# Kernel tuning notes

Hardware: AMD Instinct MI355X
Metric: run time of the kernel (lower is better)

## Reference

```python
import jax, jax.numpy as jnp
import numpy as np


def setup_inputs() -> dict:
    key = jax.random.key(0)
    ks = jax.random.split(key, 9)
    B, C, PF = 4, 256, 4096
    C8 = C // 8
    scale_qk = 1.0 / np.sqrt(C)
    return {
        "x": jax.random.normal(ks[0], (B, C, PF), dtype=jnp.float32),
        "xh1": jax.random.normal(ks[1], (B, C, PF), dtype=jnp.float32),
        "xl1": jax.random.normal(ks[2], (B, C, PF), dtype=jnp.float32),
        "Wq": jax.random.normal(ks[3], (C8, C), dtype=jnp.float32) * scale_qk,
        "bq": jnp.zeros((C8,), dtype=jnp.float32),
        "Wk": jax.random.normal(ks[4], (C8, C), dtype=jnp.float32) * scale_qk,
        "bk": jnp.zeros((C8,), dtype=jnp.float32),
        "Wv": jax.random.normal(ks[5], (C, C), dtype=jnp.float32) * scale_qk,
        "bv": jnp.zeros((C,), dtype=jnp.float32),
        "gamma1": jnp.array([0.5], dtype=jnp.float32),
        "gamma2": jnp.array([0.5], dtype=jnp.float32),
    }


def reference(x, xh1, xl1, Wq, bq, Wk, bk, Wv, bv, gamma1, gamma2):
    # x, xh1, xl1: (B, C, N) with N = H*W. Conv1x1 == channel-wise linear,
    # so the (B,C,H,W) reshape in the original is a no-op for the math.
    q = jnp.einsum("oc,bcn->bon", Wq, x) + bq[None, :, None]   # (B, C/8, N)
    k = jnp.einsum("oc,bcn->bon", Wk, x) + bk[None, :, None]   # (B, C/8, N)
    # energy[b, n, m] = q[:, :, n] . k[:, :, m]  (NO 1/sqrt(d) scale, as in source)
    energy = jnp.einsum("bcn,bcm->bnm", q, k)                  # (B, N, N)
    attention = jax.nn.softmax(energy, axis=-1)                # softmax over keys m
    vh = jnp.einsum("oc,bcn->bon", Wv, xh1) + bv[None, :, None]  # (B, C, N)
    vl = jnp.einsum("oc,bcn->bon", Wv, xl1) + bv[None, :, None]  # (B, C, N)
    # out = V @ attention^T : out[b, c, n] = sum_m vh[b, c, m] * attention[b, n, m]
    outh = jnp.einsum("bcm,bnm->bcn", vh, attention)
    outl = jnp.einsum("bcm,bnm->bcn", vl, attention)
    outh = xh1 * (gamma1 * outh)
    outl = xl1 * (gamma2 * outl)
    return outh, outl
```

## Files before the change

kernel.cpp:

```cpp
#include <hip/hip_runtime.h>
#include <math.h>

#define B_  4
#define C_  256
#define C8_ 32
#define N_  4096
#define NT_ 128

typedef __attribute__((ext_vector_type(8))) short          bf16x8;
typedef __attribute__((ext_vector_type(8))) unsigned short us8;
typedef __attribute__((ext_vector_type(4))) unsigned short us4;
typedef __attribute__((ext_vector_type(4))) float          f32x4;

__device__ inline unsigned short f2bf(float f) {
    unsigned u = __float_as_uint(f);
    u += 0x7FFFu + ((u >> 16) & 1u);
    return (unsigned short)(u >> 16);
}
__device__ inline void splitbf(float v, unsigned short& h, unsigned short& l) {
    unsigned short hh = f2bf(v);
    float hf = __uint_as_float((unsigned)hh << 16);
    h = hh; l = f2bf(v - hf);
}
__device__ inline bf16x8 asb(us8 v) { return __builtin_bit_cast(bf16x8, v); }

template<int MODE>
__global__ __launch_bounds__(256, 4) void proj_k(
    const float* __restrict__ Xa, const float* __restrict__ Xb,
    const float* __restrict__ Wa, const float* __restrict__ Wb,
    const float* __restrict__ ba, const float* __restrict__ bb,
    float* __restrict__ qt, float* __restrict__ ktt,
    unsigned short* __restrict__ vtc)
{
    __shared__ unsigned short XsH[32][66], XsL[32][66];
    __shared__ unsigned short WsH[64][40], WsL[64][40];

    const int m0 = blockIdx.x * 64;
    int b, s, cc0;
    const float* xptr;
    if (MODE == 0) { b = blockIdx.z; s = 0; cc0 = 0;
                     xptr = Xa + (size_t)b * C_ * N_; }
    else           { b = blockIdx.z & 3; s = blockIdx.z >> 2; cc0 = blockIdx.y * 64;
                     xptr = (s ? Xb : Xa) + (size_t)b * C_ * N_; }

    const int t = threadIdx.x;
    const int w = t >> 6, lane = t & 63, lr = lane & 15, ls = lane >> 4;

    f32x4 acc[4];
    #pragma unroll
    for (int i = 0; i < 4; ++i) acc[i] = (f32x4){0.f, 0.f, 0.f, 0.f};

    const int skk = t >> 3, smo = (t & 7) * 8;
    const int scc = t >> 2, sko = (t & 3) * 8;
    const float* wrow;
    if (MODE == 0) wrow = (scc < 32) ? (Wa + (size_t)scc * C_) : (Wb + (size_t)(scc - 32) * C_);
    else           wrow = Wa + (size_t)(cc0 + scc) * C_;

    for (int k0 = 0; k0 < C_; k0 += 32) {
        __syncthreads();
        {
            const float* src = xptr + (size_t)(k0 + skk) * N_ + m0 + smo;
            f32x4 a = *(const f32x4*)src, c = *(const f32x4*)(src + 4);
            unsigned short h[8], l[8];
            splitbf(a[0],h[0],l[0]); splitbf(a[1],h[1],l[1]);
            splitbf(a[2],h[2],l[2]); splitbf(a[3],h[3],l[3]);
            splitbf(c[0],h[4],l[4]); splitbf(c[1],h[5],l[5]);
            splitbf(c[2],h[6],l[6]); splitbf(c[3],h[7],l[7]);
            unsigned* dh = (unsigned*)&XsH[skk][smo];
            unsigned* dl = (unsigned*)&XsL[skk][smo];
            #pragma unroll
            for (int i = 0; i < 4; ++i) {
                dh[i] = (unsigned)h[2*i] | ((unsigned)h[2*i+1] << 16);
                dl[i] = (unsigned)l[2*i] | ((unsigned)l[2*i+1] << 16);
            }
        }
        {
            f32x4 a = *(const f32x4*)(wrow + k0 + sko);
            f32x4 c = *(const f32x4*)(wrow + k0 + sko + 4);
            us8 h, l; unsigned short hh, ll;
            splitbf(a[0],hh,ll); h[0]=hh; l[0]=ll;
            splitbf(a[1],hh,ll); h[1]=hh; l[1]=ll;
            splitbf(a[2],hh,ll); h[2]=hh; l[2]=ll;
            splitbf(a[3],hh,ll); h[3]=hh; l[3]=ll;
            splitbf(c[0],hh,ll); h[4]=hh; l[4]=ll;
            splitbf(c[1],hh,ll); h[5]=hh; l[5]=ll;
            splitbf(c[2],hh,ll); h[6]=hh; l[6]=ll;
            splitbf(c[3],hh,ll); h[7]=hh; l[7]=ll;
            *(us8*)&WsH[scc][sko] = h;
            *(us8*)&WsL[scc][sko] = l;
        }
        __syncthreads();
        us8 ahu, alu;
        #pragma unroll
        for (int j = 0; j < 8; ++j) {
            ahu[j] = XsH[ls*8 + j][w*16 + lr];
            alu[j] = XsL[ls*8 + j][w*16 + lr];
        }
        bf16x8 ah = asb(ahu), al = asb(alu);
        #pragma unroll
        for (int at = 0; at < 4; ++at) {
            bf16x8 bh = asb(*(const us8*)&WsH[at*16 + lr][ls*8]);
            bf16x8 bl = asb(*(const us8*)&WsL[at*16 + lr][ls*8]);
            acc[at] = __builtin_amdgcn_mfma_f32_16x16x32_bf16(ah, bh, acc[at], 0, 0, 0);
            acc[at] = __builtin_amdgcn_mfma_f32_16x16x32_bf16(ah, bl, acc[at], 0, 0, 0);
            acc[at] = __builtin_amdgcn_mfma_f32_16x16x32_bf16(al, bh, acc[at], 0, 0, 0);
        }
    }

    const int mrow = m0 + w*16 + ls*4;
    if (MODE == 0) {
        #pragma unroll
        for (int at = 0; at < 4; ++at) {
            const int cc = at*16 + lr;
            if (at < 2) {
                const float bia = ba[cc];
                #pragma unroll
                for (int r = 0; r < 4; ++r)
                    qt[((size_t)b * N_ + mrow + r) * C8_ + cc] = acc[at][r] + bia;
            } else {
                const float bia = bb[cc - 32];
                f32x4 o;
                #pragma unroll
                for (int r = 0; r < 4; ++r) o[r] = acc[at][r] + bia;
                *(f32x4*)&ktt[((size_t)b * C8_ + cc - 32) * N_ + mrow] = o;
            }
        }
    } else {
        #pragma unroll
        for (int at = 0; at < 4; ++at) {
            const int cc = cc0 + at*16 + lr;
            const float bia = ba[cc];
            us4 o;
            #pragma unroll
            for (int r = 0; r < 4; ++r) o[r] = f2bf(acc[at][r] + bia);
            *(us4*)&vtc[((size_t)b * 512 + s * 256 + cc) * N_ + mrow] = o;
        }
    }
}

__global__ __launch_bounds__(512, 4) void pv_k(
    const float* __restrict__ qt, const float* __restrict__ ktt,
    const unsigned short* __restrict__ vtc,
    const float* __restrict__ xh1, const float* __restrict__ xl1,
    const float* __restrict__ g1, const float* __restrict__ g2,
    float* __restrict__ out)
{
    __shared__ unsigned short KsH[2][32][34];
    __shared__ unsigned short KsL[2][32][34];
    __shared__ unsigned short Ps[32][40];
    __shared__ float          Zpart[2][32];

    const int orig = blockIdx.x;
    const int wg   = (orig & 7) * 64 + (orig >> 3);
    const int b    = wg >> 7;
    const int n0   = (wg & 127) * 32;

    const int t = threadIdx.x, w = t >> 6, lane = t & 63;
    const int lr = lane & 15, ls = lane >> 4;
    const int wn = w * 64;
    const bool ew = (w < 4);
    const int rt = (w >> 1) & 1, mt = w & 1;

    bf16x8 qh = {}, ql = {};
    if (ew) {
        const float* qrow = qt + ((size_t)b * N_ + n0 + rt*16 + lr) * C8_ + ls*8;
        f32x4 q0 = *(const f32x4*)qrow, q1 = *(const f32x4*)(qrow + 4);
        us8 hu, lu; unsigned short hh, ll;
        splitbf(q0[0],hh,ll); hu[0]=hh; lu[0]=ll;
        splitbf(q0[1],hh,ll); hu[1]=hh; lu[1]=ll;
        splitbf(q0[2],hh,ll); hu[2]=hh; lu[2]=ll;
        splitbf(q0[3],hh,ll); hu[3]=hh; lu[3]=ll;
        splitbf(q1[0],hh,ll); hu[4]=hh; lu[4]=ll;
        splitbf(q1[1],hh,ll); hu[5]=hh; lu[5]=ll;
        splitbf(q1[2],hh,ll); hu[6]=hh; lu[6]=ll;
        splitbf(q1[3],hh,ll); hu[7]=hh; lu[7]=ll;
        qh = asb(hu); ql = asb(lu);
    }

    f32x4 acc[2][4];
    #pragma unroll
    for (int i = 0; i < 2; ++i)
        #pragma unroll
        for (int j = 0; j < 4; ++j) acc[i][j] = (f32x4){0.f, 0.f, 0.f, 0.f};
    float zreg[4] = {0.f, 0.f, 0.f, 0.f};

    const unsigned short* vbase = vtc + (size_t)b * 512 * N_;
    const unsigned short* vp0 = vbase + (size_t)(wn +  0 + lr) * N_ + ls*8;
    const unsigned short* vp1 = vbase + (size_t)(wn + 16 + lr) * N_ + ls*8;
    const unsigned short* vp2 = vbase + (size_t)(wn + 32 + lr) * N_ + ls*8;
    const unsigned short* vp3 = vbase + (size_t)(wn + 48 + lr) * N_ + ls*8;

    const int ts = t - 256, kc = (ts & 255) >> 3, kmq = (ts & 7) * 4;
    const float* kptr = ktt + ((size_t)b * C8_ + kc) * N_ + kmq;

    us8 vA0, vA1, vA2, vA3, vB0, vB1, vB2, vB3;

    if (!ew) {
        f32x4 kv = *(const f32x4*)kptr;
        unsigned short h0,h1,h2,h3,l0,l1,l2,l3;
        splitbf(kv[0],h0,l0); splitbf(kv[1],h1,l1);
        splitbf(kv[2],h2,l2); splitbf(kv[3],h3,l3);
        unsigned* dh = (unsigned*)&KsH[0][kc][kmq];
        unsigned* dl = (unsigned*)&KsL[0][kc][kmq];
        dh[0] = (unsigned)h0 | ((unsigned)h1 << 16);
        dh[1] = (unsigned)h2 | ((unsigned)h3 << 16);
        dl[0] = (unsigned)l0 | ((unsigned)l1 << 16);
        dl[1] = (unsigned)l2 | ((unsigned)l3 << 16);
    }
    vA0 = *(const us8*)vp0; vA1 = *(const us8*)vp1;
    vA2 = *(const us8*)vp2; vA3 = *(const us8*)vp3;
    __syncthreads();

    auto body = [&](int CUR, int NXT, us8& VC0, us8& VC1, us8& VC2, us8& VC3,
                    us8& VN0, us8& VN1, us8& VN2, us8& VN3, int TILE) {
        const int tn = TILE + 1;
        f32x4 kreg;
        if (tn < NT_) {
            VN0 = *(const us8*)(vp0 + tn*32);
            VN1 = *(const us8*)(vp1 + tn*32);
            VN2 = *(const us8*)(vp2 + tn*32);
            VN3 = *(const us8*)(vp3 + tn*32);
            if (!ew) kreg = *(const f32x4*)(kptr + tn*32);
        }
        if (ew) {
            us8 khu, klu;
            #pragma unroll
            for (int j = 0; j < 8; ++j) {
                khu[j] = KsH[CUR][ls*8 + j][mt*16 + lr];
                klu[j] = KsL[CUR][ls*8 + j][mt*16 + lr];
            }
            bf16x8 kh = asb(khu), kl = asb(klu);
            f32x4 ea = (f32x4){0.f, 0.f, 0.f, 0.f};
            ea = __builtin_amdgcn_mfma_f32_16x16x32_bf16(qh, kh, ea, 0, 0, 0);
            ea = __builtin_amdgcn_mfma_f32_16x16x32_bf16(qh, kl, ea, 0, 0, 0);
            ea = __builtin_amdgcn_mfma_f32_16x16x32_bf16(ql, kh, ea, 0, 0, 0);
            #pragma unroll
            for (int r = 0; r < 4; ++r) {
                float pe = __expf(ea[r] - 20.f);
                zreg[r] += pe;
                Ps[rt*16 + ls*4 + r][mt*16 + lr] = f2bf(pe);
            }
        }
        __syncthreads();
        {
            bf16x8 pa0 = asb(*(const us8*)&Ps[lr][ls*8]);
            bf16x8 pa1 = asb(*(const us8*)&Ps[16 + lr][ls*8]);
            bf16x8 v0 = asb(VC0), v1 = asb(VC1), v2 = asb(VC2), v3 = asb(VC3);
            acc[0][0] = __builtin_amdgcn_mfma_f32_16x16x32_bf16(pa0, v0, acc[0][0], 0,0,0);
            acc[1][0] = __builtin_amdgcn_mfma_f32_16x16x32_bf16(pa1, v0, acc[1][0], 0,0,0);
            acc[0][1] = __builtin_amdgcn_mfma_f32_16x16x32_bf16(pa0, v1, acc[0][1], 0,0,0);
            acc[1][1] = __builtin_amdgcn_mfma_f32_16x16x32_bf16(pa1, v1, acc[1][1], 0,0,0);
            acc[0][2] = __builtin_amdgcn_mfma_f32_16x16x32_bf16(pa0, v2, acc[0][2], 0,0,0);
            acc[1][2] = __builtin_amdgcn_mfma_f32_16x16x32_bf16(pa1, v2, acc[1][2], 0,0,0);
            acc[0][3] = __builtin_amdgcn_mfma_f32_16x16x32_bf16(pa0, v3, acc[0][3], 0,0,0);
            acc[1][3] = __builtin_amdgcn_mfma_f32_16x16x32_bf16(pa1, v3, acc[1][3], 0,0,0);
        }
        if (tn < NT_ && !ew) {
            unsigned short h0,h1,h2,h3,l0,l1,l2,l3;
            splitbf(kreg[0],h0,l0); splitbf(kreg[1],h1,l1);
            splitbf(kreg[2],h2,l2); splitbf(kreg[3],h3,l3);
            unsigned* dh = (unsigned*)&KsH[NXT][kc][kmq];
            unsigned* dl = (unsigned*)&KsL[NXT][kc][kmq];
            dh[0] = (unsigned)h0 | ((unsigned)h1 << 16);
            dh[1] = (unsigned)h2 | ((unsigned)h3 << 16);
            dl[0] = (unsigned)l0 | ((unsigned)l1 << 16);
            dl[1] = (unsigned)l2 | ((unsigned)l3 << 16);
        }
        __syncthreads();
    };

    for (int tile = 0; tile < NT_; tile += 2) {
        body(0, 1, vA0, vA1, vA2, vA3, vB0, vB1, vB2, vB3, tile);
        body(1, 0, vB0, vB1, vB2, vB3, vA0, vA1, vA2, vA3, tile + 1);
    }

    if (ew) {
        #pragma unroll
        for (int r = 0; r < 4; ++r) {
            float z = zreg[r];
            z += __shfl_xor(z, 1, 16); z += __shfl_xor(z, 2, 16);
            z += __shfl_xor(z, 4, 16); z += __shfl_xor(z, 8, 16);
            if (lr == 0) Zpart[mt][rt*16 + ls*4 + r] = z;
        }
    }
    __syncthreads();

    float rzf[2][4];
    #pragma unroll
    for (int fi = 0; fi < 2; ++fi)
        #pragma unroll
        for (int r = 0; r < 4; ++r) {
            const int row = fi*16 + ls*4 + r;
            rzf[fi][r] = 1.f / (Zpart[0][row] + Zpart[1][row]);
        }
    const float g1v = g1[0], g2v = g2[0];
    #pragma unroll
    for (int fi = 0; fi < 2; ++fi) {
        const int nb = fi*16 + ls*4;
        #pragma unroll
        for (int fj = 0; fj < 4; ++fj) {
            const int cc = wn + fj*16 + lr;
            const int st = cc >> 8;
            const float  gv = st ? g2v : g1v;
            const float* xg = st ? xl1 : xh1;
            float* og = out + (st ? (size_t)B_ * C_ * N_ : (size_t)0);
            const size_t base = ((size_t)b * C_ + (cc & 255)) * N_ + n0 + nb;
            f32x4 xv = *(const f32x4*)(xg + base);
            f32x4 o;
            #pragma unroll
            for (int r = 0; r < 4; ++r)
                o[r] = xv[r] * (gv * (acc[fi][fj][r] * rzf[fi][r]));
            *(f32x4*)(og + base) = o;
        }
    }
}

extern "C" void kernel_launch(void* const* d_in, const int* in_sizes, int n_in,
                              void* d_out, int out_size, void* d_ws, size_t ws_size,
                              hipStream_t stream)
{
    const float* x   = (const float*)d_in[0];
    const float* xh1 = (const float*)d_in[1];
    const float* xl1 = (const float*)d_in[2];
    const float* Wq  = (const float*)d_in[3];
    const float* bq  = (const float*)d_in[4];
    const float* Wk  = (const float*)d_in[5];
    const float* bk  = (const float*)d_in[6];
    const float* Wv  = (const float*)d_in[7];
    const float* bv  = (const float*)d_in[8];
    const float* g1  = (const float*)d_in[9];
    const float* g2  = (const float*)d_in[10];
    float* out = (float*)d_out;

    char* pws = (char*)d_ws;
    float* qt  = (float*)pws;                 pws += (size_t)B_ * N_ * C8_ * 4;
    float* ktt = (float*)pws;                 pws += (size_t)B_ * N_ * C8_ * 4;
    unsigned short* vtc = (unsigned short*)pws;

    proj_k<0><<<dim3(N_ / 64, 1, B_),     256, 0, stream>>>(
        x, nullptr, Wq, Wk, bq, bk, qt, ktt, nullptr);
    proj_k<1><<<dim3(N_ / 64, 4, B_ * 2), 256, 0, stream>>>(
        xh1, xl1, Wv, nullptr, bv, nullptr, nullptr, nullptr, vtc);
    pv_k<<<dim3(512), 512, 0, stream>>>(qt, ktt, vtc, xh1, xl1, g1, g2, out);
}
```

Before: 388.7 us.

## Restructure attention kernel to 64-key tiles with all warps computing energies

The attention kernel now processes 64 keys per tile instead of 32. All eight warps compute QK energies directly from a row-major K buffer held in registers, replacing the split where half the warps staged K into shared memory. This halves the number of barrier pairs and drops the K staging through LDS, but every warp now re-splits K to bf16 and 4-way partial softmax sums must be combined. The V projection now covers 128 output channels per block, and X tiles are packed hi/lo into one 32-bit shared array. The batch-to-XCD block mapping is also changed.

```diff
diff --git a/kernel.cpp b/kernel.cpp
--- a/kernel.cpp
+++ b/kernel.cpp
@@ -5,12 +5,13 @@
 #define C_  256
 #define C8_ 32
 #define N_  4096
-#define NT_ 128
+#define NT64_ 64
 
 typedef __attribute__((ext_vector_type(8))) short          bf16x8;
 typedef __attribute__((ext_vector_type(8))) unsigned short us8;
 typedef __attribute__((ext_vector_type(4))) unsigned short us4;
 typedef __attribute__((ext_vector_type(4))) float          f32x4;
+typedef __attribute__((ext_vector_type(4))) unsigned       u32x4;
 
 __device__ inline unsigned short f2bf(float f) {
     unsigned u = __float_as_uint(f);
@@ -21,6 +22,10 @@
     unsigned short hh = f2bf(v);
     float hf = __uint_as_float((unsigned)hh << 16);
     h = hh; l = f2bf(v - hf);
+}
+__device__ inline unsigned packbf(float v) {
+    unsigned short h, l; splitbf(v, h, l);
+    return (unsigned)h | ((unsigned)l << 16);
 }
 __device__ inline bf16x8 asb(us8 v) { return __builtin_bit_cast(bf16x8, v); }
 
@@ -29,29 +34,32 @@
     const float* __restrict__ Xa, const float* __restrict__ Xb,
     const float* __restrict__ Wa, const float* __restrict__ Wb,
     const float* __restrict__ ba, const float* __restrict__ bb,
-    float* __restrict__ qt, float* __restrict__ ktt,
+    float* __restrict__ qt, float* __restrict__ kt,
     unsigned short* __restrict__ vtc)
 {
-    __shared__ unsigned short XsH[32][66], XsL[32][66];
-    __shared__ unsigned short WsH[64][40], WsL[64][40];
-
+    __shared__ unsigned       XsP[32][68];
+    __shared__ unsigned short WsH[(MODE ? 128 : 64)][40];
+    __shared__ unsigned short WsL[(MODE ? 128 : 64)][40];
+
+    constexpr int CCT = MODE ? 8 : 4;
     const int m0 = blockIdx.x * 64;
     int b, s, cc0;
     const float* xptr;
     if (MODE == 0) { b = blockIdx.z; s = 0; cc0 = 0;
                      xptr = Xa + (size_t)b * C_ * N_; }
-    else           { b = blockIdx.z & 3; s = blockIdx.z >> 2; cc0 = blockIdx.y * 64;
+    else           { b = blockIdx.z & 3; s = blockIdx.z >> 2; cc0 = blockIdx.y * 128;
                      xptr = (s ? Xb : Xa) + (size_t)b * C_ * N_; }
 
     const int t = threadIdx.x;
     const int w = t >> 6, lane = t & 63, lr = lane & 15, ls = lane >> 4;
 
-    f32x4 acc[4];
-    #pragma unroll
-    for (int i = 0; i < 4; ++i) acc[i] = (f32x4){0.f, 0.f, 0.f, 0.f};
+    f32x4 acc[CCT];
+    #pragma unroll
+    for (int i = 0; i < CCT; ++i) acc[i] = (f32x4){0.f, 0.f, 0.f, 0.f};
 
     const int skk = t >> 3, smo = (t & 7) * 8;
-    const int scc = t >> 2, sko = (t & 3) * 8;
+    const int scc = MODE ? (t >> 1) : (t >> 2);
+    const int sko = MODE ? ((t & 1) * 16) : ((t & 3) * 8);
     const float* wrow;
     if (MODE == 0) wrow = (scc < 32) ? (Wa + (size_t)scc * C_) : (Wb + (size_t)(scc - 32) * C_);
     else           wrow = Wa + (size_t)(cc0 + scc) * C_;
@@ -61,44 +69,42 @@
         {
             const float* src = xptr + (size_t)(k0 + skk) * N_ + m0 + smo;
             f32x4 a = *(const f32x4*)src, c = *(const f32x4*)(src + 4);
-            unsigned short h[8], l[8];
-            splitbf(a[0],h[0],l[0]); splitbf(a[1],h[1],l[1]);
-            splitbf(a[2],h[2],l[2]); splitbf(a[3],h[3],l[3]);
-            splitbf(c[0],h[4],l[4]); splitbf(c[1],h[5],l[5]);
-            splitbf(c[2],h[6],l[6]); splitbf(c[3],h[7],l[7]);
-            unsigned* dh = (unsigned*)&XsH[skk][smo];
-            unsigned* dl = (unsigned*)&XsL[skk][smo];
-            #pragma unroll
-            for (int i = 0; i < 4; ++i) {
-                dh[i] = (unsigned)h[2*i] | ((unsigned)h[2*i+1] << 16);
-                dl[i] = (unsigned)l[2*i] | ((unsigned)l[2*i+1] << 16);
-            }
+            u32x4 p0, p1;
+            p0[0]=packbf(a[0]); p0[1]=packbf(a[1]); p0[2]=packbf(a[2]); p0[3]=packbf(a[3]);
+            p1[0]=packbf(c[0]); p1[1]=packbf(c[1]); p1[2]=packbf(c[2]); p1[3]=packbf(c[3]);
+            *(u32x4*)&XsP[skk][smo]     = p0;
+            *(u32x4*)&XsP[skk][smo + 4] = p1;
         }
         {
-            f32x4 a = *(const f32x4*)(wrow + k0 + sko);
-            f32x4 c = *(const f32x4*)(wrow + k0 + sko + 4);
-            us8 h, l; unsigned short hh, ll;
-            splitbf(a[0],hh,ll); h[0]=hh; l[0]=ll;
-            splitbf(a[1],hh,ll); h[1]=hh; l[1]=ll;
-            splitbf(a[2],hh,ll); h[2]=hh; l[2]=ll;
-            splitbf(a[3],hh,ll); h[3]=hh; l[3]=ll;
-            splitbf(c[0],hh,ll); h[4]=hh; l[4]=ll;
-            splitbf(c[1],hh,ll); h[5]=hh; l[5]=ll;
-            splitbf(c[2],hh,ll); h[6]=hh; l[6]=ll;
-            splitbf(c[3],hh,ll); h[7]=hh; l[7]=ll;
-            *(us8*)&WsH[scc][sko] = h;
-            *(us8*)&WsL[scc][sko] = l;
+            const int nk = MODE ? 16 : 8;
+            #pragma unroll
+            for (int q = 0; q < nk / 8; ++q) {
+                f32x4 a = *(const f32x4*)(wrow + k0 + sko + q * 8);
+                f32x4 c = *(const f32x4*)(wrow + k0 + sko + q * 8 + 4);
+                us8 h, l; unsigned short hh, ll;
+                splitbf(a[0],hh,ll); h[0]=hh; l[0]=ll;
+                splitbf(a[1],hh,ll); h[1]=hh; l[1]=ll;
+                splitbf(a[2],hh,ll); h[2]=hh; l[2]=ll;
+                splitbf(a[3],hh,ll); h[3]=hh; l[3]=ll;
+                splitbf(c[0],hh,ll); h[4]=hh; l[4]=ll;
+                splitbf(c[1],hh,ll); h[5]=hh; l[5]=ll;
+                splitbf(c[2],hh,ll); h[6]=hh; l[6]=ll;
+                splitbf(c[3],hh,ll); h[7]=hh; l[7]=ll;
+                *(us8*)&WsH[scc][sko + q * 8] = h;
+                *(us8*)&WsL[scc][sko + q * 8] = l;
+            }
         }
         __syncthreads();
         us8 ahu, alu;
         #pragma unroll
         for (int j = 0; j < 8; ++j) {
-            ahu[j] = XsH[ls*8 + j][w*16 + lr];
-            alu[j] = XsL[ls*8 + j][w*16 + lr];
+            unsigned v = XsP[ls*8 + j][w*16 + lr];
+            ahu[j] = (unsigned short)v;
+            alu[j] = (unsigned short)(v >> 16);
         }
         bf16x8 ah = asb(ahu), al = asb(alu);
         #pragma unroll
-        for (int at = 0; at < 4; ++at) {
+        for (int at = 0; at < CCT; ++at) {
             bf16x8 bh = asb(*(const us8*)&WsH[at*16 + lr][ls*8]);
             bf16x8 bl = asb(*(const us8*)&WsL[at*16 + lr][ls*8]);
             acc[at] = __builtin_amdgcn_mfma_f32_16x16x32_bf16(ah, bh, acc[at], 0, 0, 0);
@@ -110,7 +116,7 @@
     const int mrow = m0 + w*16 + ls*4;
     if (MODE == 0) {
         #pragma unroll
-        for (int at = 0; at < 4; ++at) {
+        for (int at = 0; at < CCT; ++at) {
             const int cc = at*16 + lr;
             if (at < 2) {
                 const float bia = ba[cc];
@@ -119,15 +125,14 @@
                     qt[((size_t)b * N_ + mrow + r) * C8_ + cc] = acc[at][r] + bia;
             } else {
                 const float bia = bb[cc - 32];
-                f32x4 o;
                 #pragma unroll
-                for (int r = 0; r < 4; ++r) o[r] = acc[at][r] + bia;
-                *(f32x4*)&ktt[((size_t)b * C8_ + cc - 32) * N_ + mrow] = o;
+                for (int r = 0; r < 4; ++r)
+                    kt[((size_t)b * N_ + mrow + r) * C8_ + (cc - 32)] = acc[at][r] + bia;
             }
         }
     } else {
         #pragma unroll
-        for (int at = 0; at < 4; ++at) {
+        for (int at = 0; at < CCT; ++at) {
             const int cc = cc0 + at*16 + lr;
             const float bia = ba[cc];
             us4 o;
@@ -139,30 +144,29 @@
 }
 
 __global__ __launch_bounds__(512, 4) void pv_k(
-    const float* __restrict__ qt, const float* __restrict__ ktt,
+    const float* __restrict__ qt, const float* __restrict__ kt,
     const unsigned short* __restrict__ vtc,
     const float* __restrict__ xh1, const float* __restrict__ xl1,
     const float* __restrict__ g1, const float* __restrict__ g2,
     float* __restrict__ out)
 {
-    __shared__ unsigned short KsH[2][32][34];
-    __shared__ unsigned short KsL[2][32][34];
-    __shared__ unsigned short Ps[32][40];
-    __shared__ float          Zpart[2][32];
-
-    const int orig = blockIdx.x;
-    const int wg   = (orig & 7) * 64 + (orig >> 3);
-    const int b    = wg >> 7;
-    const int n0   = (wg & 127) * 32;
+    __shared__ unsigned short Ps[32][72];
+    __shared__ float Zpart[4][32];
+
+    const int o      = blockIdx.x;
+    const int xcd    = o & 7;
+    const int b      = xcd >> 1;
+    const int rowblk = (o >> 3) + (xcd & 1) * 64;
+    const int n0     = rowblk * 32;
 
     const int t = threadIdx.x, w = t >> 6, lane = t & 63;
     const int lr = lane & 15, ls = lane >> 4;
     const int wn = w * 64;
-    const bool ew = (w < 4);
-    const int rt = (w >> 1) & 1, mt = w & 1;
-
-    bf16x8 qh = {}, ql = {};
-    if (ew) {
+    const int rt = w >> 2;
+    const int mt = w & 3;
+
+    bf16x8 qh, ql;
+    {
         const float* qrow = qt + ((size_t)b * N_ + n0 + rt*16 + lr) * C8_ + ls*8;
         f32x4 q0 = *(const f32x4*)qrow, q1 = *(const f32x4*)(qrow + 4);
         us8 hu, lu; unsigned short hh, ll;
@@ -184,56 +188,41 @@
         for (int j = 0; j < 4; ++j) acc[i][j] = (f32x4){0.f, 0.f, 0.f, 0.f};
     float zreg[4] = {0.f, 0.f, 0.f, 0.f};
 
+    const float* kp = kt + ((size_t)b * N_ + mt*16 + lr) * C8_ + ls*8;
     const unsigned short* vbase = vtc + (size_t)b * 512 * N_;
-    const unsigned short* vp0 = vbase + (size_t)(wn +  0 + lr) * N_ + ls*8;
-    const unsigned short* vp1 = vbase + (size_t)(wn + 16 + lr) * N_ + ls*8;
-    const unsigned short* vp2 = vbase + (size_t)(wn + 32 + lr) * N_ + ls*8;
-    const unsigned short* vp3 = vbase + (size_t)(wn + 48 + lr) * N_ + ls*8;
-
-    const int ts = t - 256, kc = (ts & 255) >> 3, kmq = (ts & 7) * 4;
-    const float* kptr = ktt + ((size_t)b * C8_ + kc) * N_ + kmq;
-
-    us8 vA0, vA1, vA2, vA3, vB0, vB1, vB2, vB3;
-
-    if (!ew) {
-        f32x4 kv = *(const f32x4*)kptr;
-        unsigned short h0,h1,h2,h3,l0,l1,l2,l3;
-        splitbf(kv[0],h0,l0); splitbf(kv[1],h1,l1);
-        splitbf(kv[2],h2,l2); splitbf(kv[3],h3,l3);
-        unsigned* dh = (unsigned*)&KsH[0][kc][kmq];
-        unsigned* dl = (unsigned*)&KsL[0][kc][kmq];
-        dh[0] = (unsigned)h0 | ((unsigned)h1 << 16);
-        dh[1] = (unsigned)h2 | ((unsigned)h3 << 16);
-        dl[0] = (unsigned)l0 | ((unsigned)l1 << 16);
-        dl[1] = (unsigned)l2 | ((unsigned)l3 << 16);
-    }
-    vA0 = *(const us8*)vp0; vA1 = *(const us8*)vp1;
-    vA2 = *(const us8*)vp2; vA3 = *(const us8*)vp3;
-    __syncthreads();
-
-    auto body = [&](int CUR, int NXT, us8& VC0, us8& VC1, us8& VC2, us8& VC3,
-                    us8& VN0, us8& VN1, us8& VN2, us8& VN3, int TILE) {
-        const int tn = TILE + 1;
-        f32x4 kreg;
-        if (tn < NT_) {
-            VN0 = *(const us8*)(vp0 + tn*32);
-            VN1 = *(const us8*)(vp1 + tn*32);
-            VN2 = *(const us8*)(vp2 + tn*32);
-            VN3 = *(const us8*)(vp3 + tn*32);
-            if (!ew) kreg = *(const f32x4*)(kptr + tn*32);
-        }
-        if (ew) {
-            us8 khu, klu;
-            #pragma unroll
-            for (int j = 0; j < 8; ++j) {
-                khu[j] = KsH[CUR][ls*8 + j][mt*16 + lr];
-                klu[j] = KsL[CUR][ls*8 + j][mt*16 + lr];
-            }
+    const unsigned short* vp[4];
+    #pragma unroll
+    for (int fj = 0; fj < 4; ++fj)
+        vp[fj] = vbase + (size_t)(wn + fj*16 + lr) * N_ + ls*8;
+
+    f32x4 kc0 = *(const f32x4*)kp, kc1 = *(const f32x4*)(kp + 4);
+    us8 v[4][2];
+    #pragma unroll
+    for (int fj = 0; fj < 4; ++fj) {
+        v[fj][0] = *(const us8*)(vp[fj]);
+        v[fj][1] = *(const us8*)(vp[fj] + 32);
+    }
+
+    for (int tile = 0; tile < NT64_; ++tile) {
+        {
+            us8 khu, klu; unsigned short hh, ll;
+            splitbf(kc0[0],hh,ll); khu[0]=hh; klu[0]=ll;
+            splitbf(kc0[1],hh,ll); khu[1]=hh; klu[1]=ll;
+            splitbf(kc0[2],hh,ll); khu[2]=hh; klu[2]=ll;
+            splitbf(kc0[3],hh,ll); khu[3]=hh; klu[3]=ll;
+            splitbf(kc1[0],hh,ll); khu[4]=hh; klu[4]=ll;
+            splitbf(kc1[1],hh,ll); khu[5]=hh; klu[5]=ll;
+            splitbf(kc1[2],hh,ll); khu[6]=hh; klu[6]=ll;
+            splitbf(kc1[3],hh,ll); khu[7]=hh; klu[7]=ll;
             bf16x8 kh = asb(khu), kl = asb(klu);
             f32x4 ea = (f32x4){0.f, 0.f, 0.f, 0.f};
             ea = __builtin_amdgcn_mfma_f32_16x16x32_bf16(qh, kh, ea, 0, 0, 0);
             ea = __builtin_amdgcn_mfma_f32_16x16x32_bf16(qh, kl, ea, 0, 0, 0);
             ea = __builtin_amdgcn_mfma_f32_16x16x32_bf16(ql, kh, ea, 0, 0, 0);
+            if (tile + 1 < NT64_) {
+                kc0 = *(const f32x4*)(kp + (size_t)(tile + 1) * 64 * C8_);
+                kc1 = *(const f32x4*)(kp + (size_t)(tile + 1) * 64 * C8_ + 4);
+            }
             #pragma unroll
             for (int r = 0; r < 4; ++r) {
                 float pe = __expf(ea[r] - 20.f);
@@ -243,60 +232,51 @@
         }
         __syncthreads();
         {
-            bf16x8 pa0 = asb(*(const us8*)&Ps[lr][ls*8]);
-            bf16x8 pa1 = asb(*(const us8*)&Ps[16 + lr][ls*8]);
-            bf16x8 v0 = asb(VC0), v1 = asb(VC1), v2 = asb(VC2), v3 = asb(VC3);
-            acc[0][0] = __builtin_amdgcn_mfma_f32_16x16x32_bf16(pa0, v0, acc[0][0], 0,0,0);
-            acc[1][0] = __builtin_amdgcn_mfma_f32_16x16x32_bf16(pa1, v0, acc[1][0], 0,0,0);
-            acc[0][1] = __builtin_amdgcn_mfma_f32_16x16x32_bf16(pa0, v1, acc[0][1], 0,0,0);
-            acc[1][1] = __builtin_amdgcn_mfma_f32_16x16x32_bf16(pa1, v1, acc[1][1], 0,0,0);
-            acc[0][2] = __builtin_amdgcn_mfma_f32_16x16x32_bf16(pa0, v2, acc[0][2], 0,0,0);
-            acc[1][2] = __builtin_amdgcn_mfma_f32_16x16x32_bf16(pa1, v2, acc[1][2], 0,0,0);
-            acc[0][3] = __builtin_amdgcn_mfma_f32_16x16x32_bf16(pa0, v3, acc[0][3], 0,0,0);
-            acc[1][3] = __builtin_amdgcn_mfma_f32_16x16x32_bf16(pa1, v3, acc[1][3], 0,0,0);
-        }
-        if (tn < NT_ && !ew) {
-            unsigned short h0,h1,h2,h3,l0,l1,l2,l3;
-            splitbf(kreg[0],h0,l0); splitbf(kreg[1],h1,l1);
-            splitbf(kreg[2],h2,l2); splitbf(kreg[3],h3,l3);
-            unsigned* dh = (unsigned*)&KsH[NXT][kc][kmq];
-            unsigned* dl = (unsigned*)&KsL[NXT][kc][kmq];
-            dh[0] = (unsigned)h0 | ((unsigned)h1 << 16);
-            dh[1] = (unsigned)h2 | ((unsigned)h3 << 16);
-            dl[0] = (unsigned)l0 | ((unsigned)l1 << 16);
-            dl[1] = (unsigned)l2 | ((unsigned)l3 << 16);
+            bf16x8 pa00 = asb(*(const us8*)&Ps[lr][ls*8]);
+            bf16x8 pa01 = asb(*(const us8*)&Ps[lr][32 + ls*8]);
+            bf16x8 pa10 = asb(*(const us8*)&Ps[16 + lr][ls*8]);
+            bf16x8 pa11 = asb(*(const us8*)&Ps[16 + lr][32 + ls*8]);
+            #pragma unroll
+            for (int fj = 0; fj < 4; ++fj) {
+                acc[0][fj] = __builtin_amdgcn_mfma_f32_16x16x32_bf16(pa00, asb(v[fj][0]), acc[0][fj], 0,0,0);
+                acc[1][fj] = __builtin_amdgcn_mfma_f32_16x16x32_bf16(pa10, asb(v[fj][0]), acc[1][fj], 0,0,0);
+                acc[0][fj] = __builtin_amdgcn_mfma_f32_16x16x32_bf16(pa01, asb(v[fj][1]), acc[0][fj], 0,0,0);
+                acc[1][fj] = __builtin_amdgcn_mfma_f32_16x16x32_bf16(pa11, asb(v[fj][1]), acc[1][fj], 0,0,0);
+            }
+            if (tile + 1 < NT64_) {
+                const int mo = (tile + 1) * 64;
+                #pragma unroll
+                for (int fj = 0; fj < 4; ++fj) {
+                    v[fj][0] = *(const us8*)(vp[fj] + mo);
+                    v[fj][1] = *(const us8*)(vp[fj] + mo + 32);
+                }
+            }
         }
         __syncthreads();
-    };
-
-    for (int tile = 0; tile < NT_; tile += 2) {
-        body(0, 1, vA0, vA1, vA2, vA3, vB0, vB1, vB2, vB3, tile);
-        body(1, 0, vB0, vB1, vB2, vB3, vA0, vA1, vA2, vA3, tile + 1);
-    }
-
-    if (ew) {
+    }
+
+    #pragma unroll
+    for (int r = 0; r < 4; ++r) {
+        float z = zreg[r];
+        z += __shfl_xor(z, 1, 16); z += __shfl_xor(z, 2, 16);
+        z += __shfl_xor(z, 4, 16); z += __shfl_xor(z, 8, 16);
+        if (lr == 0) Zpart[mt][rt*16 + ls*4 + r] = z;
+    }
+    __syncthreads();
+
+    float rzf[2][4];
+    #pragma unroll
+    for (int rh = 0; rh < 2; ++rh)
         #pragma unroll
         for (int r = 0; r < 4; ++r) {
-            float z = zreg[r];
-            z += __shfl_xor(z, 1, 16); z += __shfl_xor(z, 2, 16);
-            z += __shfl_xor(z, 4, 16); z += __shfl_xor(z, 8, 16);
-            if (lr == 0) Zpart[mt][rt*16 + ls*4 + r] = z;
-        }
-    }
-    __syncthreads();
-
-    float rzf[2][4];
-    #pragma unroll
-    for (int fi = 0; fi < 2; ++fi)
-        #pragma unroll
-        for (int r = 0; r < 4; ++r) {
-            const int row = fi*16 + ls*4 + r;
-            rzf[fi][r] = 1.f / (Zpart[0][row] + Zpart[1][row]);
-        }
+            const int row = rh*16 + ls*4 + r;
+            rzf[rh][r] = 1.f / (Zpart[0][row] + Zpart[1][row] + Zpart[2][row] + Zpart[3][row]);
+        }
+
     const float g1v = g1[0], g2v = g2[0];
     #pragma unroll
-    for (int fi = 0; fi < 2; ++fi) {
-        const int nb = fi*16 + ls*4;
+    for (int rh = 0; rh < 2; ++rh) {
+        const int nb = rh*16 + ls*4;
         #pragma unroll
         for (int fj = 0; fj < 4; ++fj) {
             const int cc = wn + fj*16 + lr;
@@ -306,11 +286,11 @@
             float* og = out + (st ? (size_t)B_ * C_ * N_ : (size_t)0);
             const size_t base = ((size_t)b * C_ + (cc & 255)) * N_ + n0 + nb;
             f32x4 xv = *(const f32x4*)(xg + base);
-            f32x4 o;
+            f32x4 ov;
             #pragma unroll
             for (int r = 0; r < 4; ++r)
-                o[r] = xv[r] * (gv * (acc[fi][fj][r] * rzf[fi][r]));
-            *(f32x4*)(og + base) = o;
+                ov[r] = xv[r] * (gv * (acc[rh][fj][r] * rzf[rh][r]));
+            *(f32x4*)(og + base) = ov;
         }
     }
 }
@@ -333,13 +313,13 @@
     float* out = (float*)d_out;
 
     char* pws = (char*)d_ws;
-    float* qt  = (float*)pws;                 pws += (size_t)B_ * N_ * C8_ * 4;
-    float* ktt = (float*)pws;                 pws += (size_t)B_ * N_ * C8_ * 4;
+    float* qt = (float*)pws;                  pws += (size_t)B_ * N_ * C8_ * 4;
+    float* kt = (float*)pws;                  pws += (size_t)B_ * N_ * C8_ * 4;
     unsigned short* vtc = (unsigned short*)pws;
 
     proj_k<0><<<dim3(N_ / 64, 1, B_),     256, 0, stream>>>(
-        x, nullptr, Wq, Wk, bq, bk, qt, ktt, nullptr);
-    proj_k<1><<<dim3(N_ / 64, 4, B_ * 2), 256, 0, stream>>>(
+        x, nullptr, Wq, Wk, bq, bk, qt, kt, nullptr);
+    proj_k<1><<<dim3(N_ / 64, 2, B_ * 2), 256, 0, stream>>>(
         xh1, xl1, Wv, nullptr, bv, nullptr, nullptr, nullptr, vtc);
-    pv_k<<<dim3(512), 512, 0, stream>>>(qt, ktt, vtc, xh1, xl1, g1, g2, out);
-}
+    pv_k<<<dim3(512), 512, 0, stream>>>(qt, kt, vtc, xh1, xl1, g1, g2, out);
+}
```

Result: slower. 425.7 us (+9.5%).
